# Performance work log

Hardware: AMD Instinct MI355X
Metric: run time of the kernel (lower is better)

The kernel has to match this reference:

```python
import jax, jax.numpy as jnp
import numpy as np

B, S, D, E, H = 65536, 4, 128, 128, 4
HD = E // H
EPS = 1e-5


def setup_inputs() -> dict:
    key = jax.random.key(0)
    ks = jax.random.split(key, 20)
    sc = 0.05
    return {
        'h0': jax.random.normal(ks[0], (B, D), jnp.float32),
        'h1': jax.random.normal(ks[1], (B, D), jnp.float32),
        'h2': jax.random.normal(ks[2], (B, D), jnp.float32),
        'h3': jax.random.normal(ks[3], (B, D), jnp.float32),
        'proj_w': jax.random.normal(ks[4], (S, D, E), jnp.float32) * sc,
        'proj_b': jax.random.normal(ks[5], (S, E), jnp.float32) * sc,
        'ctx_w': jax.random.normal(ks[6], (E,), jnp.float32) * sc,
        'ctx_b': jax.random.normal(ks[7], (), jnp.float32) * sc,
        'in_proj_w': jax.random.normal(ks[8], (E, 3 * E), jnp.float32) * sc,
        'in_proj_b': jax.random.normal(ks[9], (3 * E,), jnp.float32) * sc,
        'out_w': jax.random.normal(ks[10], (E, E), jnp.float32) * sc,
        'out_b': jax.random.normal(ks[11], (E,), jnp.float32) * sc,
        'gate_w': jax.random.normal(ks[12], (2 * E, E), jnp.float32) * sc,
        'gate_b': jax.random.normal(ks[13], (E,), jnp.float32) * sc,
        'pool_w': jax.random.normal(ks[14], (E,), jnp.float32) * sc,
        'pool_b': jax.random.normal(ks[15], (), jnp.float32) * sc,
        'ln_g': jnp.ones((E,), jnp.float32),
        'ln_b': jnp.zeros((E,), jnp.float32),
    }


def reference(h0, h1, h2, h3, proj_w, proj_b, ctx_w, ctx_b, in_proj_w, in_proj_b,
              out_w, out_b, gate_w, gate_b, pool_w, pool_b, ln_g, ln_b):
    hs = jnp.stack([h0, h1, h2, h3], axis=1)                      # [B,S,D]
    x = jnp.einsum('bsd,sde->bse', hs, proj_w) + proj_b           # [B,S,E]
    # context attention over sources
    cw = jax.nn.softmax(x @ ctx_w + ctx_b, axis=1)                # [B,S]
    context = jnp.einsum('bse,bs->be', x, cw)                     # [B,E]
    # single-query MHA: query=context, keys/vals=x
    wq, wk, wv = jnp.split(in_proj_w, 3, axis=1)
    bq, bk, bv = jnp.split(in_proj_b, 3)
    q = (context @ wq + bq).reshape(B, H, HD)
    k = (x @ wk + bk).reshape(B, S, H, HD)
    v = (x @ wv + bv).reshape(B, S, H, HD)
    scores = jnp.einsum('bhd,bshd->bhs', q, k) / jnp.sqrt(jnp.float32(HD))
    attn = jax.nn.softmax(scores, axis=-1)                        # [B,H,S]
    o = jnp.einsum('bhs,bshd->bhd', attn, v).reshape(B, E)
    attn_out = o @ out_w + out_b                                  # [B,E]
    attn_weights = jnp.mean(attn, axis=1)[:, None, :]             # [B,1,S] (avg heads)
    ao = jnp.broadcast_to(attn_out[:, None, :], (B, S, E))
    gate_in = jnp.concatenate([x, ao], axis=-1)                   # [B,S,2E]
    g = jax.nn.sigmoid(gate_in @ gate_w + gate_b)                 # [B,S,E]
    fused = g * ao + (1.0 - g) * x
    mu = fused.mean(axis=-1, keepdims=True)
    var = fused.var(axis=-1, keepdims=True)
    fused = (fused - mu) * jax.lax.rsqrt(var + EPS) * ln_g + ln_b
    pw = jax.nn.softmax(fused @ pool_w + pool_b, axis=1)          # [B,S]
    pooled = jnp.einsum('bse,bs->be', fused, pw)                  # [B,E]
    return pooled, attn_weights, g
```

## Files before the change

kernel.cpp:

```cpp
#include <hip/hip_runtime.h>
#include <hip/hip_bf16.h>

typedef unsigned short u16;
typedef unsigned int   u32;
typedef short  short8 __attribute__((ext_vector_type(8)));
typedef float  f32x4  __attribute__((ext_vector_type(4)));

#define NB   65536
#define ROWS 64
#define XP   136
#define OFF1 ((size_t)NB * 128)
#define OFF2 (OFF1 + (size_t)NB * 4)

__device__ __forceinline__ u16 f2bf(float f) {
  union { float f; u32 u; } v; v.f = f;
  return (u16)((v.u + 0x7FFFu + ((v.u >> 16) & 1u)) >> 16);
}
__device__ __forceinline__ float bf2f(u32 bits16) {
  union { u32 u; float f; } v; v.u = bits16 << 16; return v.f;
}
__device__ __forceinline__ u32 pk2(float a, float b) {
  return (u32)f2bf(a) | ((u32)f2bf(b) << 16);
}

__global__ void pack_w(const float* __restrict__ proj_w,
                       const float* __restrict__ in_proj_w,
                       const float* __restrict__ out_w,
                       const float* __restrict__ gate_w,
                       u16* __restrict__ wp) {
  int t = blockIdx.x * 256 + threadIdx.x;
  if (t >= 10 * 16384) return;
  int w = t >> 14, i = t & 16383;
  int nt = i >> 11, kt = (i >> 9) & 3, ln = (i >> 3) & 63, j = i & 7;
  int k = kt * 32 + ((ln >> 4) << 3) + j;
  int n = (nt << 4) + (ln & 15);
  float v;
  if (w < 4)       v = proj_w[((size_t)w << 14) + (k << 7) + n];
  else if (w < 7)  v = in_proj_w[k * 384 + ((w - 4) << 7) + n];
  else if (w == 7) v = out_w[(k << 7) + n];
  else             v = gate_w[(((w - 8) << 7) + k) * 128 + n];
  wp[t] = f2bf(v);
}

__device__ __forceinline__ short8 bfrag(const u16* __restrict__ wp, int w, int nt, int kt, int lane) {
  return *(const short8*)(wp + ((size_t)w << 14) + (size_t)((((nt << 2) + kt) << 6) + lane) * 8);
}

struct AF { short8 a[4]; };
__device__ __forceinline__ AF loadA(const u16 (*Ab)[XP], int row, int lgrp) {
  AF r;
  #pragma unroll
  for (int kt = 0; kt < 4; ++kt)
    r.a[kt] = *(const short8*)&Ab[row][kt * 32 + (lgrp << 3)];
  return r;
}
__device__ __forceinline__ f32x4 mmK128(const AF& A, const u16* __restrict__ wp, int w,
                                        int nt, int lane, float bias) {
  f32x4 acc = {bias, bias, bias, bias};
  #pragma unroll
  for (int kt = 0; kt < 4; ++kt)
    acc = __builtin_amdgcn_mfma_f32_16x16x32_bf16(A.a[kt], bfrag(wp, w, nt, kt, lane), acc, 0, 0, 0);
  return acc;
}

__global__ __launch_bounds__(256) void fused_k(
    const float* __restrict__ h0, const float* __restrict__ h1,
    const float* __restrict__ h2, const float* __restrict__ h3,
    const u16* __restrict__ wp,
    const float* __restrict__ proj_b, const float* __restrict__ ctx_w,
    const float* __restrict__ in_proj_b, const float* __restrict__ out_b,
    const float* __restrict__ gate_b, const float* __restrict__ pool_w,
    const float* __restrict__ ln_g, const float* __restrict__ ln_b,
    float* __restrict__ out) {
  __shared__ __align__(16) u16 xls[4][ROWS][XP];
  __shared__ __align__(16) u16 aux[ROWS][XP];
  __shared__ __align__(16) u16 aob[ROWS][XP];
  __shared__ float lgt[4][ROWS];
  __shared__ float scf[4][ROWS][4];
  __shared__ float lnr[ROWS][4][2];
  __shared__ float lgp[4][ROWS];
  __shared__ float lnw[3][128];

  const int tid  = threadIdx.x;
  const int lane = tid & 63;
  const int wr   = (tid >> 6) << 4;
  const int r0   = blockIdx.x * ROWS;
  const int lrow = lane & 15;
  const int lgrp = lane >> 4;
  const int crow0 = lgrp << 2;

  if (tid < 128) { lnw[0][tid] = pool_w[tid]; lnw[1][tid] = ln_g[tid]; lnw[2][tid] = ln_b[tid]; }

  const float* hp[4] = {h0, h1, h2, h3};

  #pragma unroll
  for (int s = 0; s < 4; ++s) {
    const float* __restrict__ hs = hp[s];
    #pragma unroll
    for (int i = 0; i < 8; ++i) {
      int f4 = i * 256 + tid;
      int row = f4 >> 5, c0 = (f4 & 31) << 2;
      const float4 v = *(const float4*)(hs + ((size_t)(r0 + row) << 7) + c0);
      *(uint2*)&aux[row][c0] = make_uint2(pk2(v.x, v.y), pk2(v.z, v.w));
    }
    __syncthreads();
    AF A = loadA(aux, wr + lrow, lgrp);
    float lp0 = 0, lp1 = 0, lp2 = 0, lp3 = 0;
    #pragma unroll
    for (int nt = 0; nt < 8; ++nt) {
      int n = (nt << 4) + lrow;
      f32x4 acc = mmK128(A, wp, s, nt, lane, proj_b[(s << 7) + n]);
      float cwn = ctx_w[n];
      lp0 += acc[0] * cwn; lp1 += acc[1] * cwn; lp2 += acc[2] * cwn; lp3 += acc[3] * cwn;
      xls[s][wr + crow0 + 0][n] = f2bf(acc[0]);
      xls[s][wr + crow0 + 1][n] = f2bf(acc[1]);
      xls[s][wr + crow0 + 2][n] = f2bf(acc[2]);
      xls[s][wr + crow0 + 3][n] = f2bf(acc[3]);
    }
    #pragma unroll
    for (int m = 1; m < 16; m <<= 1) {
      lp0 += __shfl_xor(lp0, m); lp1 += __shfl_xor(lp1, m);
      lp2 += __shfl_xor(lp2, m); lp3 += __shfl_xor(lp3, m);
    }
    if (lrow == 0) {
      lgt[s][wr + crow0 + 0] = lp0; lgt[s][wr + crow0 + 1] = lp1;
      lgt[s][wr + crow0 + 2] = lp2; lgt[s][wr + crow0 + 3] = lp3;
    }
    __syncthreads();
  }

  if (tid < ROWS) {
    float l0 = lgt[0][tid], l1 = lgt[1][tid], l2 = lgt[2][tid], l3 = lgt[3][tid];
    float mx = fmaxf(fmaxf(l0, l1), fmaxf(l2, l3));
    float e0 = __expf(l0 - mx), e1 = __expf(l1 - mx), e2 = __expf(l2 - mx), e3 = __expf(l3 - mx);
    float inv = 1.f / (e0 + e1 + e2 + e3);
    lgt[0][tid] = e0 * inv; lgt[1][tid] = e1 * inv; lgt[2][tid] = e2 * inv; lgt[3][tid] = e3 * inv;
  }
  __syncthreads();

  #pragma unroll
  for (int i = 0; i < 8; ++i) {
    int e4 = i * 256 + tid;
    int row = e4 >> 5, c0 = (e4 & 31) << 2;
    float c0v = 0, c1v = 0, c2v = 0, c3v = 0;
    #pragma unroll
    for (int s = 0; s < 4; ++s) {
      float cw = lgt[s][row];
      uint2 d = *(const uint2*)&xls[s][row][c0];
      c0v += cw * bf2f(d.x & 0xffff); c1v += cw * bf2f(d.x >> 16);
      c2v += cw * bf2f(d.y & 0xffff); c3v += cw * bf2f(d.y >> 16);
    }
    *(uint2*)&aux[row][c0] = make_uint2(pk2(c0v, c1v), pk2(c2v, c3v));
  }
  __syncthreads();

  {
    AF A = loadA(aux, wr + lrow, lgrp);
    #pragma unroll
    for (int nt = 0; nt < 8; ++nt) {
      int n = (nt << 4) + lrow;
      f32x4 acc = mmK128(A, wp, 4, nt, lane, in_proj_b[n]);
      #pragma unroll
      for (int j = 0; j < 4; ++j) aob[wr + crow0 + j][n] = f2bf(acc[j]);
    }
  }
  __syncthreads();

  #pragma unroll
  for (int s = 0; s < 4; ++s) {
    float sc[4][4] = {};
    AF A = loadA(xls[s], wr + lrow, lgrp);
    #pragma unroll
    for (int nt = 0; nt < 8; ++nt) {
      int n = (nt << 4) + lrow;
      f32x4 acc = mmK128(A, wp, 5, nt, lane, in_proj_b[128 + n]);
      #pragma unroll
      for (int j = 0; j < 4; ++j)
        sc[j][nt >> 1] += acc[j] * bf2f((u32)aob[wr + crow0 + j][n]);
    }
    #pragma unroll
    for (int m = 1; m < 16; m <<= 1)
      #pragma unroll
      for (int j = 0; j < 4; ++j)
        #pragma unroll
        for (int h = 0; h < 4; ++h)
          sc[j][h] += __shfl_xor(sc[j][h], m);
    #pragma unroll
    for (int h = 0; h < 4; ++h)
      if (lrow == h) {
        #pragma unroll
        for (int j = 0; j < 4; ++j) scf[s][wr + crow0 + j][h] = sc[j][h];
      }
  }
  __syncthreads();

  {
    int row = tid >> 2, h = tid & 3;
    const float scale = 0.17677669529663687f;
    float l0 = scf[0][row][h] * scale, l1 = scf[1][row][h] * scale;
    float l2 = scf[2][row][h] * scale, l3 = scf[3][row][h] * scale;
    float mx = fmaxf(fmaxf(l0, l1), fmaxf(l2, l3));
    float e0 = __expf(l0 - mx), e1 = __expf(l1 - mx), e2 = __expf(l2 - mx), e3 = __expf(l3 - mx);
    float inv = 1.f / (e0 + e1 + e2 + e3);
    scf[0][row][h] = e0 * inv; scf[1][row][h] = e1 * inv;
    scf[2][row][h] = e2 * inv; scf[3][row][h] = e3 * inv;
  }
  __syncthreads();
  {
    int row = tid >> 2, s = tid & 3;
    float m = 0.25f * (scf[s][row][0] + scf[s][row][1] + scf[s][row][2] + scf[s][row][3]);
    out[OFF1 + ((size_t)(r0 + row) << 2) + s] = m;
  }

  {
    float oa[8][4] = {};
    #pragma unroll
    for (int s = 0; s < 4; ++s) {
      AF A = loadA(xls[s], wr + lrow, lgrp);
      float aw[4][4];
      #pragma unroll
      for (int j = 0; j < 4; ++j)
        #pragma unroll
        for (int h = 0; h < 4; ++h) aw[j][h] = scf[s][wr + crow0 + j][h];
      #pragma unroll
      for (int nt = 0; nt < 8; ++nt) {
        int n = (nt << 4) + lrow;
        f32x4 acc = mmK128(A, wp, 6, nt, lane, in_proj_b[256 + n]);
        #pragma unroll
        for (int j = 0; j < 4; ++j) oa[nt][j] += aw[j][nt >> 1] * acc[j];
      }
    }
    #pragma unroll
    for (int nt = 0; nt < 8; ++nt) {
      int n = (nt << 4) + lrow;
      #pragma unroll
      for (int j = 0; j < 4; ++j) aux[wr + crow0 + j][n] = f2bf(oa[nt][j]);
    }
  }
  __syncthreads();

  {
    AF A = loadA(aux, wr + lrow, lgrp);
    #pragma unroll
    for (int nt = 0; nt < 8; ++nt) {
      int n = (nt << 4) + lrow;
      f32x4 acc = mmK128(A, wp, 7, nt, lane, out_b[n]);
      #pragma unroll
      for (int j = 0; j < 4; ++j) aob[wr + crow0 + j][n] = f2bf(acc[j]);
    }
  }
  __syncthreads();

  #pragma unroll 1
  for (int s = 0; s < 4; ++s) {
    {
      AF Ax = loadA(xls[s], wr + lrow, lgrp);
      AF Aa = loadA(aob, wr + lrow, lgrp);
      #pragma unroll
      for (int nt = 0; nt < 8; ++nt) {
        int n = (nt << 4) + lrow;
        float b = gate_b[n];
        f32x4 acc = {b, b, b, b};
        #pragma unroll
        for (int kt = 0; kt < 4; ++kt)
          acc = __builtin_amdgcn_mfma_f32_16x16x32_bf16(Ax.a[kt], bfrag(wp, 8, nt, kt, lane), acc, 0, 0, 0);
        #pragma unroll
        for (int kt = 0; kt < 4; ++kt)
          acc = __builtin_amdgcn_mfma_f32_16x16x32_bf16(Aa.a[kt], bfrag(wp, 9, nt, kt, lane), acc, 0, 0, 0);
        #pragma unroll
        for (int j = 0; j < 4; ++j) {
          float g = 1.f / (1.f + __expf(-acc[j]));
          out[OFF2 + (((size_t)(r0 + wr + crow0 + j) << 2) + s) * 128 + n] = g;
          aux[wr + crow0 + j][n] = f2bf(g);
        }
      }
    }
    __syncthreads();
    int row = tid >> 2, p = tid & 3, e0 = (tid & 3) << 5;
    float sum = 0, ss = 0;
    #pragma unroll
    for (int c = 0; c < 8; ++c) {
      int e = e0 + (c << 2);
      uint2 gd = *(const uint2*)&aux[row][e];
      uint2 ad = *(const uint2*)&aob[row][e];
      uint2 xd = *(const uint2*)&xls[s][row][e];
      float g0 = bf2f(gd.x & 0xffff), g1 = bf2f(gd.x >> 16), g2 = bf2f(gd.y & 0xffff), g3 = bf2f(gd.y >> 16);
      float a0 = bf2f(ad.x & 0xffff), a1 = bf2f(ad.x >> 16), a2 = bf2f(ad.y & 0xffff), a3 = bf2f(ad.y >> 16);
      float x0 = bf2f(xd.x & 0xffff), x1 = bf2f(xd.x >> 16), x2 = bf2f(xd.y & 0xffff), x3 = bf2f(xd.y >> 16);
      float f0 = g0 * a0 + (1.f - g0) * x0, f1 = g1 * a1 + (1.f - g1) * x1;
      float f2 = g2 * a2 + (1.f - g2) * x2, f3 = g3 * a3 + (1.f - g3) * x3;
      sum += f0 + f1 + f2 + f3;
      ss  += f0 * f0 + f1 * f1 + f2 * f2 + f3 * f3;
      *(uint2*)&xls[s][row][e] = make_uint2(pk2(f0, f1), pk2(f2, f3));
    }
    lnr[row][p][0] = sum; lnr[row][p][1] = ss;
    __syncthreads();
    float ts  = lnr[row][0][0] + lnr[row][1][0] + lnr[row][2][0] + lnr[row][3][0];
    float tss = lnr[row][0][1] + lnr[row][1][1] + lnr[row][2][1] + lnr[row][3][1];
    float mean = ts * 0.0078125f;
    float var  = tss * 0.0078125f - mean * mean;
    float rstd = rsqrtf(var + 1e-5f);
    float pp = 0;
    #pragma unroll
    for (int c = 0; c < 8; ++c) {
      int e = e0 + (c << 2);
      uint2 fd = *(const uint2*)&xls[s][row][e];
      float f0 = bf2f(fd.x & 0xffff), f1 = bf2f(fd.x >> 16), f2 = bf2f(fd.y & 0xffff), f3 = bf2f(fd.y >> 16);
      f0 = (f0 - mean) * rstd * lnw[1][e + 0] + lnw[2][e + 0];
      f1 = (f1 - mean) * rstd * lnw[1][e + 1] + lnw[2][e + 1];
      f2 = (f2 - mean) * rstd * lnw[1][e + 2] + lnw[2][e + 2];
      f3 = (f3 - mean) * rstd * lnw[1][e + 3] + lnw[2][e + 3];
      pp += f0 * lnw[0][e] + f1 * lnw[0][e + 1] + f2 * lnw[0][e + 2] + f3 * lnw[0][e + 3];
      *(uint2*)&xls[s][row][e] = make_uint2(pk2(f0, f1), pk2(f2, f3));
    }
    scf[0][row][p] = pp;
    __syncthreads();
    if (p == 0)
      lgp[s][row] = scf[0][row][0] + scf[0][row][1] + scf[0][row][2] + scf[0][row][3];
    __syncthreads();
  }

  if (tid < ROWS) {
    float l0 = lgp[0][tid], l1 = lgp[1][tid], l2 = lgp[2][tid], l3 = lgp[3][tid];
    float mx = fmaxf(fmaxf(l0, l1), fmaxf(l2, l3));
    float e0 = __expf(l0 - mx), e1 = __expf(l1 - mx), e2 = __expf(l2 - mx), e3 = __expf(l3 - mx);
    float inv = 1.f / (e0 + e1 + e2 + e3);
    lgp[0][tid] = e0 * inv; lgp[1][tid] = e1 * inv; lgp[2][tid] = e2 * inv; lgp[3][tid] = e3 * inv;
  }
  __syncthreads();
  #pragma unroll
  for (int i = 0; i < 8; ++i) {
    int e4 = i * 256 + tid;
    int row = e4 >> 5, c0 = (e4 & 31) << 2;
    float p0 = lgp[0][row], p1 = lgp[1][row], p2 = lgp[2][row], p3 = lgp[3][row];
    float r0v = 0, r1v = 0, r2v = 0, r3v = 0;
    #pragma unroll
    for (int s = 0; s < 4; ++s) {
      float pw = (s == 0) ? p0 : (s == 1) ? p1 : (s == 2) ? p2 : p3;
      uint2 d = *(const uint2*)&xls[s][row][c0];
      r0v += pw * bf2f(d.x & 0xffff); r1v += pw * bf2f(d.x >> 16);
      r2v += pw * bf2f(d.y & 0xffff); r3v += pw * bf2f(d.y >> 16);
    }
    float4 o4; o4.x = r0v; o4.y = r1v; o4.z = r2v; o4.w = r3v;
    *(float4*)(out + ((size_t)(r0 + row) << 7) + c0) = o4;
  }
}

extern "C" void kernel_launch(void* const* d_in, const int* in_sizes, int n_in,
                              void* d_out, int out_size, void* d_ws, size_t ws_size,
                              hipStream_t stream) {
  const float* h0        = (const float*)d_in[0];
  const float* h1        = (const float*)d_in[1];
  const float* h2        = (const float*)d_in[2];
  const float* h3        = (const float*)d_in[3];
  const float* proj_w    = (const float*)d_in[4];
  const float* proj_b    = (const float*)d_in[5];
  const float* ctx_w     = (const float*)d_in[6];
  const float* in_proj_w = (const float*)d_in[8];
  const float* in_proj_b = (const float*)d_in[9];
  const float* out_w     = (const float*)d_in[10];
  const float* out_b     = (const float*)d_in[11];
  const float* gate_w    = (const float*)d_in[12];
  const float* gate_b    = (const float*)d_in[13];
  const float* pool_w    = (const float*)d_in[14];
  const float* ln_g      = (const float*)d_in[16];
  const float* ln_b      = (const float*)d_in[17];
  u16* wp = (u16*)d_ws;

  pack_w<<<640, 256, 0, stream>>>(proj_w, in_proj_w, out_w, gate_w, wp);
  fused_k<<<NB / ROWS, 256, 0, stream>>>(h0, h1, h2, h3, wp,
                                         proj_b, ctx_w, in_proj_b, out_b, gate_b,
                                         pool_w, ln_g, ln_b, (float*)d_out);
}
```

Before: 211.3 us.

## Split output columns across two waves on 16-row tiles, keep operands in registers

The fused kernel now works on 16 rows per block with 128 threads. The two waves split the 128 output columns instead of the rows, so each weight fragment is loaded once and reused across the four sources. Source activations, q, and attention output stay in registers, and the gate, residual mix and layernorm are done on MFMA accumulators with cross-lane reductions rather than through shared-memory round trips. This cuts LDS traffic and barriers and may raise occupancy. In exchange, each block re-reads the full weight set for only 16 rows, and the code adds more cross-wave reductions and register pressure.

```diff
diff --git a/kernel.cpp b/kernel.cpp
--- a/kernel.cpp
+++ b/kernel.cpp
@@ -7,7 +7,7 @@
 typedef float  f32x4  __attribute__((ext_vector_type(4)));
 
 #define NB   65536
-#define ROWS 64
+#define ROWS 16
 #define XP   136
 #define OFF1 ((size_t)NB * 128)
 #define OFF2 (OFF1 + (size_t)NB * 4)
@@ -21,6 +21,11 @@
 }
 __device__ __forceinline__ u32 pk2(float a, float b) {
   return (u32)f2bf(a) | ((u32)f2bf(b) << 16);
+}
+__device__ __forceinline__ float red16(float v) {
+  v += __shfl_xor(v, 1); v += __shfl_xor(v, 2);
+  v += __shfl_xor(v, 4); v += __shfl_xor(v, 8);
+  return v;
 }
 
 __global__ void pack_w(const float* __restrict__ proj_w,
@@ -55,15 +60,15 @@
   return r;
 }
 __device__ __forceinline__ f32x4 mmK128(const AF& A, const u16* __restrict__ wp, int w,
-                                        int nt, int lane, float bias) {
+                                        int ntg, int lane, float bias) {
   f32x4 acc = {bias, bias, bias, bias};
   #pragma unroll
   for (int kt = 0; kt < 4; ++kt)
-    acc = __builtin_amdgcn_mfma_f32_16x16x32_bf16(A.a[kt], bfrag(wp, w, nt, kt, lane), acc, 0, 0, 0);
+    acc = __builtin_amdgcn_mfma_f32_16x16x32_bf16(A.a[kt], bfrag(wp, w, ntg, kt, lane), acc, 0, 0, 0);
   return acc;
 }
 
-__global__ __launch_bounds__(256) void fused_k(
+__global__ __launch_bounds__(128, 3) void fused_k(
     const float* __restrict__ h0, const float* __restrict__ h1,
     const float* __restrict__ h2, const float* __restrict__ h3,
     const u16* __restrict__ wp,
@@ -75,21 +80,19 @@
   __shared__ __align__(16) u16 xls[4][ROWS][XP];
   __shared__ __align__(16) u16 aux[ROWS][XP];
   __shared__ __align__(16) u16 aob[ROWS][XP];
-  __shared__ float lgt[4][ROWS];
+  __shared__ float lgt[4][2][ROWS];
   __shared__ float scf[4][ROWS][4];
-  __shared__ float lnr[ROWS][4][2];
-  __shared__ float lgp[4][ROWS];
-  __shared__ float lnw[3][128];
-
-  const int tid  = threadIdx.x;
-  const int lane = tid & 63;
-  const int wr   = (tid >> 6) << 4;
-  const int r0   = blockIdx.x * ROWS;
-  const int lrow = lane & 15;
-  const int lgrp = lane >> 4;
+  __shared__ float lnr[ROWS][2][2];
+  __shared__ float lgp2[4][ROWS][2];
+
+  const int tid   = threadIdx.x;
+  const int lane  = tid & 63;
+  const int wid   = tid >> 6;
+  const int nt0   = wid << 2;
+  const int r0    = blockIdx.x * ROWS;
+  const int lrow  = lane & 15;
+  const int lgrp  = lane >> 4;
   const int crow0 = lgrp << 2;
-
-  if (tid < 128) { lnw[0][tid] = pool_w[tid]; lnw[1][tid] = ln_g[tid]; lnw[2][tid] = ln_b[tid]; }
 
   const float* hp[4] = {h0, h1, h2, h3};
 
@@ -97,104 +100,130 @@
   for (int s = 0; s < 4; ++s) {
     const float* __restrict__ hs = hp[s];
     #pragma unroll
-    for (int i = 0; i < 8; ++i) {
-      int f4 = i * 256 + tid;
+    for (int i = 0; i < 4; ++i) {
+      int f4 = i * 128 + tid;
       int row = f4 >> 5, c0 = (f4 & 31) << 2;
       const float4 v = *(const float4*)(hs + ((size_t)(r0 + row) << 7) + c0);
-      *(uint2*)&aux[row][c0] = make_uint2(pk2(v.x, v.y), pk2(v.z, v.w));
-    }
-    __syncthreads();
-    AF A = loadA(aux, wr + lrow, lgrp);
-    float lp0 = 0, lp1 = 0, lp2 = 0, lp3 = 0;
-    #pragma unroll
-    for (int nt = 0; nt < 8; ++nt) {
-      int n = (nt << 4) + lrow;
-      f32x4 acc = mmK128(A, wp, s, nt, lane, proj_b[(s << 7) + n]);
+      *(uint2*)&xls[s][row][c0] = make_uint2(pk2(v.x, v.y), pk2(v.z, v.w));
+    }
+  }
+  __syncthreads();
+  AF Ah[4];
+  #pragma unroll
+  for (int s = 0; s < 4; ++s) Ah[s] = loadA(xls[s], lrow, lgrp);
+  __syncthreads();
+
+  #pragma unroll
+  for (int s = 0; s < 4; ++s) {
+    float lp[4] = {0.f, 0.f, 0.f, 0.f};
+    #pragma unroll
+    for (int nt = 0; nt < 4; ++nt) {
+      int ntg = nt0 + nt, n = (ntg << 4) + lrow;
+      f32x4 acc = mmK128(Ah[s], wp, s, ntg, lane, proj_b[(s << 7) + n]);
       float cwn = ctx_w[n];
-      lp0 += acc[0] * cwn; lp1 += acc[1] * cwn; lp2 += acc[2] * cwn; lp3 += acc[3] * cwn;
-      xls[s][wr + crow0 + 0][n] = f2bf(acc[0]);
-      xls[s][wr + crow0 + 1][n] = f2bf(acc[1]);
-      xls[s][wr + crow0 + 2][n] = f2bf(acc[2]);
-      xls[s][wr + crow0 + 3][n] = f2bf(acc[3]);
-    }
-    #pragma unroll
-    for (int m = 1; m < 16; m <<= 1) {
-      lp0 += __shfl_xor(lp0, m); lp1 += __shfl_xor(lp1, m);
-      lp2 += __shfl_xor(lp2, m); lp3 += __shfl_xor(lp3, m);
-    }
+      #pragma unroll
+      for (int j = 0; j < 4; ++j) {
+        lp[j] += acc[j] * cwn;
+        xls[s][crow0 + j][n] = f2bf(acc[j]);
+      }
+    }
+    #pragma unroll
+    for (int j = 0; j < 4; ++j) lp[j] = red16(lp[j]);
     if (lrow == 0) {
-      lgt[s][wr + crow0 + 0] = lp0; lgt[s][wr + crow0 + 1] = lp1;
-      lgt[s][wr + crow0 + 2] = lp2; lgt[s][wr + crow0 + 3] = lp3;
-    }
-    __syncthreads();
-  }
+      #pragma unroll
+      for (int j = 0; j < 4; ++j) lgt[s][wid][crow0 + j] = lp[j];
+    }
+  }
+  __syncthreads();
 
   if (tid < ROWS) {
-    float l0 = lgt[0][tid], l1 = lgt[1][tid], l2 = lgt[2][tid], l3 = lgt[3][tid];
+    float l0 = lgt[0][0][tid] + lgt[0][1][tid];
+    float l1 = lgt[1][0][tid] + lgt[1][1][tid];
+    float l2 = lgt[2][0][tid] + lgt[2][1][tid];
+    float l3 = lgt[3][0][tid] + lgt[3][1][tid];
     float mx = fmaxf(fmaxf(l0, l1), fmaxf(l2, l3));
     float e0 = __expf(l0 - mx), e1 = __expf(l1 - mx), e2 = __expf(l2 - mx), e3 = __expf(l3 - mx);
     float inv = 1.f / (e0 + e1 + e2 + e3);
-    lgt[0][tid] = e0 * inv; lgt[1][tid] = e1 * inv; lgt[2][tid] = e2 * inv; lgt[3][tid] = e3 * inv;
-  }
-  __syncthreads();
-
-  #pragma unroll
-  for (int i = 0; i < 8; ++i) {
-    int e4 = i * 256 + tid;
+    lgt[0][0][tid] = e0 * inv; lgt[1][0][tid] = e1 * inv;
+    lgt[2][0][tid] = e2 * inv; lgt[3][0][tid] = e3 * inv;
+  }
+  __syncthreads();
+
+  #pragma unroll
+  for (int i = 0; i < 4; ++i) {
+    int e4 = i * 128 + tid;
     int row = e4 >> 5, c0 = (e4 & 31) << 2;
-    float c0v = 0, c1v = 0, c2v = 0, c3v = 0;
+    float a0 = 0, a1 = 0, a2 = 0, a3 = 0;
     #pragma unroll
     for (int s = 0; s < 4; ++s) {
-      float cw = lgt[s][row];
+      float cw = lgt[s][0][row];
       uint2 d = *(const uint2*)&xls[s][row][c0];
-      c0v += cw * bf2f(d.x & 0xffff); c1v += cw * bf2f(d.x >> 16);
-      c2v += cw * bf2f(d.y & 0xffff); c3v += cw * bf2f(d.y >> 16);
-    }
-    *(uint2*)&aux[row][c0] = make_uint2(pk2(c0v, c1v), pk2(c2v, c3v));
-  }
-  __syncthreads();
-
+      a0 += cw * bf2f(d.x & 0xffff); a1 += cw * bf2f(d.x >> 16);
+      a2 += cw * bf2f(d.y & 0xffff); a3 += cw * bf2f(d.y >> 16);
+    }
+    *(uint2*)&aux[row][c0] = make_uint2(pk2(a0, a1), pk2(a2, a3));
+  }
+  __syncthreads();
+
+  AF Ax[4];
+  #pragma unroll
+  for (int s = 0; s < 4; ++s) Ax[s] = loadA(xls[s], lrow, lgrp);
+  float qf[4][4];
   {
-    AF A = loadA(aux, wr + lrow, lgrp);
-    #pragma unroll
-    for (int nt = 0; nt < 8; ++nt) {
-      int n = (nt << 4) + lrow;
-      f32x4 acc = mmK128(A, wp, 4, nt, lane, in_proj_b[n]);
-      #pragma unroll
-      for (int j = 0; j < 4; ++j) aob[wr + crow0 + j][n] = f2bf(acc[j]);
-    }
-  }
-  __syncthreads();
-
-  #pragma unroll
-  for (int s = 0; s < 4; ++s) {
-    float sc[4][4] = {};
-    AF A = loadA(xls[s], wr + lrow, lgrp);
-    #pragma unroll
-    for (int nt = 0; nt < 8; ++nt) {
-      int n = (nt << 4) + lrow;
-      f32x4 acc = mmK128(A, wp, 5, nt, lane, in_proj_b[128 + n]);
+    AF Ac = loadA(aux, lrow, lgrp);
+    #pragma unroll
+    for (int nt = 0; nt < 4; ++nt) {
+      int ntg = nt0 + nt, n = (ntg << 4) + lrow;
+      f32x4 acc = mmK128(Ac, wp, 4, ntg, lane, in_proj_b[n]);
+      #pragma unroll
+      for (int j = 0; j < 4; ++j) qf[nt][j] = acc[j];
+    }
+  }
+
+  {
+    float sc[4][4][2] = {};
+    #pragma unroll
+    for (int nt = 0; nt < 4; ++nt) {
+      int ntg = nt0 + nt, n = (ntg << 4) + lrow;
+      const int hh = (ntg >> 1) & 1;
+      float bk = in_proj_b[128 + n];
+      f32x4 ak[4];
+      #pragma unroll
+      for (int s = 0; s < 4; ++s) ak[s] = (f32x4){bk, bk, bk, bk};
+      #pragma unroll
+      for (int kt = 0; kt < 4; ++kt) {
+        short8 bf = bfrag(wp, 5, ntg, kt, lane);
+        #pragma unroll
+        for (int s = 0; s < 4; ++s)
+          ak[s] = __builtin_amdgcn_mfma_f32_16x16x32_bf16(Ax[s].a[kt], bf, ak[s], 0, 0, 0);
+      }
+      #pragma unroll
+      for (int s = 0; s < 4; ++s)
+        #pragma unroll
+        for (int j = 0; j < 4; ++j)
+          sc[s][j][hh] += ak[s][j] * qf[nt][j];
+    }
+    #pragma unroll
+    for (int s = 0; s < 4; ++s)
       #pragma unroll
       for (int j = 0; j < 4; ++j)
-        sc[j][nt >> 1] += acc[j] * bf2f((u32)aob[wr + crow0 + j][n]);
-    }
-    #pragma unroll
-    for (int m = 1; m < 16; m <<= 1)
-      #pragma unroll
-      for (int j = 0; j < 4; ++j)
-        #pragma unroll
-        for (int h = 0; h < 4; ++h)
-          sc[j][h] += __shfl_xor(sc[j][h], m);
-    #pragma unroll
-    for (int h = 0; h < 4; ++h)
-      if (lrow == h) {
-        #pragma unroll
-        for (int j = 0; j < 4; ++j) scf[s][wr + crow0 + j][h] = sc[j][h];
-      }
-  }
-  __syncthreads();
-
-  {
+        #pragma unroll
+        for (int hh = 0; hh < 2; ++hh)
+          sc[s][j][hh] = red16(sc[s][j][hh]);
+    #pragma unroll
+    for (int s = 0; s < 4; ++s)
+      #pragma unroll
+      for (int hh = 0; hh < 2; ++hh) {
+        int h = (wid << 1) + hh;
+        if (lrow == h) {
+          #pragma unroll
+          for (int j = 0; j < 4; ++j) scf[s][crow0 + j][h] = sc[s][j][hh];
+        }
+      }
+  }
+  __syncthreads();
+
+  if (tid < 64) {
     int row = tid >> 2, h = tid & 3;
     const float scale = 0.17677669529663687f;
     float l0 = scf[0][row][h] * scale, l1 = scf[1][row][h] * scale;
@@ -206,137 +235,161 @@
     scf[2][row][h] = e2 * inv; scf[3][row][h] = e3 * inv;
   }
   __syncthreads();
-  {
+  if (tid < 64) {
     int row = tid >> 2, s = tid & 3;
     float m = 0.25f * (scf[s][row][0] + scf[s][row][1] + scf[s][row][2] + scf[s][row][3]);
     out[OFF1 + ((size_t)(r0 + row) << 2) + s] = m;
   }
 
   {
-    float oa[8][4] = {};
+    float aw[4][4][2];
+    #pragma unroll
+    for (int s = 0; s < 4; ++s)
+      #pragma unroll
+      for (int j = 0; j < 4; ++j)
+        #pragma unroll
+        for (int hh = 0; hh < 2; ++hh)
+          aw[s][j][hh] = scf[s][crow0 + j][(wid << 1) + hh];
+    float oa[4][4] = {};
+    #pragma unroll
+    for (int nt = 0; nt < 4; ++nt) {
+      int ntg = nt0 + nt, n = (ntg << 4) + lrow;
+      const int hh = (ntg >> 1) & 1;
+      float bv = in_proj_b[256 + n];
+      f32x4 av[4];
+      #pragma unroll
+      for (int s = 0; s < 4; ++s) av[s] = (f32x4){bv, bv, bv, bv};
+      #pragma unroll
+      for (int kt = 0; kt < 4; ++kt) {
+        short8 bf = bfrag(wp, 6, ntg, kt, lane);
+        #pragma unroll
+        for (int s = 0; s < 4; ++s)
+          av[s] = __builtin_amdgcn_mfma_f32_16x16x32_bf16(Ax[s].a[kt], bf, av[s], 0, 0, 0);
+      }
+      #pragma unroll
+      for (int s = 0; s < 4; ++s)
+        #pragma unroll
+        for (int j = 0; j < 4; ++j)
+          oa[nt][j] += aw[s][j][hh] * av[s][j];
+    }
+    #pragma unroll
+    for (int nt = 0; nt < 4; ++nt) {
+      int n = ((nt0 + nt) << 4) + lrow;
+      #pragma unroll
+      for (int j = 0; j < 4; ++j) aux[crow0 + j][n] = f2bf(oa[nt][j]);
+    }
+  }
+  __syncthreads();
+
+  float aoreg[4][4];
+  {
+    AF Ao = loadA(aux, lrow, lgrp);
+    #pragma unroll
+    for (int nt = 0; nt < 4; ++nt) {
+      int ntg = nt0 + nt, n = (ntg << 4) + lrow;
+      f32x4 acc = mmK128(Ao, wp, 7, ntg, lane, out_b[n]);
+      #pragma unroll
+      for (int j = 0; j < 4; ++j) {
+        aoreg[nt][j] = acc[j];
+        aob[crow0 + j][n] = f2bf(acc[j]);
+      }
+    }
+  }
+  __syncthreads();
+
+  {
+    AF Aa = loadA(aob, lrow, lgrp);
+    float lng[4], lnb[4], pwv[4], gbv[4];
+    #pragma unroll
+    for (int nt = 0; nt < 4; ++nt) {
+      int n = ((nt0 + nt) << 4) + lrow;
+      lng[nt] = ln_g[n]; lnb[nt] = ln_b[n]; pwv[nt] = pool_w[n]; gbv[nt] = gate_b[n];
+    }
     #pragma unroll
     for (int s = 0; s < 4; ++s) {
-      AF A = loadA(xls[s], wr + lrow, lgrp);
-      float aw[4][4];
-      #pragma unroll
-      for (int j = 0; j < 4; ++j)
-        #pragma unroll
-        for (int h = 0; h < 4; ++h) aw[j][h] = scf[s][wr + crow0 + j][h];
-      #pragma unroll
-      for (int nt = 0; nt < 8; ++nt) {
-        int n = (nt << 4) + lrow;
-        f32x4 acc = mmK128(A, wp, 6, nt, lane, in_proj_b[256 + n]);
-        #pragma unroll
-        for (int j = 0; j < 4; ++j) oa[nt][j] += aw[j][nt >> 1] * acc[j];
-      }
-    }
-    #pragma unroll
-    for (int nt = 0; nt < 8; ++nt) {
-      int n = (nt << 4) + lrow;
-      #pragma unroll
-      for (int j = 0; j < 4; ++j) aux[wr + crow0 + j][n] = f2bf(oa[nt][j]);
-    }
-  }
-  __syncthreads();
-
-  {
-    AF A = loadA(aux, wr + lrow, lgrp);
-    #pragma unroll
-    for (int nt = 0; nt < 8; ++nt) {
-      int n = (nt << 4) + lrow;
-      f32x4 acc = mmK128(A, wp, 7, nt, lane, out_b[n]);
-      #pragma unroll
-      for (int j = 0; j < 4; ++j) aob[wr + crow0 + j][n] = f2bf(acc[j]);
-    }
-  }
-  __syncthreads();
-
-  #pragma unroll 1
-  for (int s = 0; s < 4; ++s) {
-    {
-      AF Ax = loadA(xls[s], wr + lrow, lgrp);
-      AF Aa = loadA(aob, wr + lrow, lgrp);
-      #pragma unroll
-      for (int nt = 0; nt < 8; ++nt) {
-        int n = (nt << 4) + lrow;
-        float b = gate_b[n];
-        f32x4 acc = {b, b, b, b};
+      float fr[4][4];
+      #pragma unroll
+      for (int nt = 0; nt < 4; ++nt) {
+        int ntg = nt0 + nt, n = (ntg << 4) + lrow;
+        f32x4 acc = {gbv[nt], gbv[nt], gbv[nt], gbv[nt]};
         #pragma unroll
         for (int kt = 0; kt < 4; ++kt)
-          acc = __builtin_amdgcn_mfma_f32_16x16x32_bf16(Ax.a[kt], bfrag(wp, 8, nt, kt, lane), acc, 0, 0, 0);
+          acc = __builtin_amdgcn_mfma_f32_16x16x32_bf16(Ax[s].a[kt], bfrag(wp, 8, ntg, kt, lane), acc, 0, 0, 0);
         #pragma unroll
         for (int kt = 0; kt < 4; ++kt)
-          acc = __builtin_amdgcn_mfma_f32_16x16x32_bf16(Aa.a[kt], bfrag(wp, 9, nt, kt, lane), acc, 0, 0, 0);
+          acc = __builtin_amdgcn_mfma_f32_16x16x32_bf16(Aa.a[kt], bfrag(wp, 9, ntg, kt, lane), acc, 0, 0, 0);
         #pragma unroll
         for (int j = 0; j < 4; ++j) {
           float g = 1.f / (1.f + __expf(-acc[j]));
-          out[OFF2 + (((size_t)(r0 + wr + crow0 + j) << 2) + s) * 128 + n] = g;
-          aux[wr + crow0 + j][n] = f2bf(g);
+          out[OFF2 + (((size_t)(r0 + crow0 + j) << 2) + s) * 128 + n] = g;
+          float xv = bf2f((u32)xls[s][crow0 + j][n]);
+          fr[nt][j] = g * aoreg[nt][j] + (1.f - g) * xv;
         }
       }
-    }
-    __syncthreads();
-    int row = tid >> 2, p = tid & 3, e0 = (tid & 3) << 5;
-    float sum = 0, ss = 0;
-    #pragma unroll
-    for (int c = 0; c < 8; ++c) {
-      int e = e0 + (c << 2);
-      uint2 gd = *(const uint2*)&aux[row][e];
-      uint2 ad = *(const uint2*)&aob[row][e];
-      uint2 xd = *(const uint2*)&xls[s][row][e];
-      float g0 = bf2f(gd.x & 0xffff), g1 = bf2f(gd.x >> 16), g2 = bf2f(gd.y & 0xffff), g3 = bf2f(gd.y >> 16);
-      float a0 = bf2f(ad.x & 0xffff), a1 = bf2f(ad.x >> 16), a2 = bf2f(ad.y & 0xffff), a3 = bf2f(ad.y >> 16);
-      float x0 = bf2f(xd.x & 0xffff), x1 = bf2f(xd.x >> 16), x2 = bf2f(xd.y & 0xffff), x3 = bf2f(xd.y >> 16);
-      float f0 = g0 * a0 + (1.f - g0) * x0, f1 = g1 * a1 + (1.f - g1) * x1;
-      float f2 = g2 * a2 + (1.f - g2) * x2, f3 = g3 * a3 + (1.f - g3) * x3;
-      sum += f0 + f1 + f2 + f3;
-      ss  += f0 * f0 + f1 * f1 + f2 * f2 + f3 * f3;
-      *(uint2*)&xls[s][row][e] = make_uint2(pk2(f0, f1), pk2(f2, f3));
-    }
-    lnr[row][p][0] = sum; lnr[row][p][1] = ss;
-    __syncthreads();
-    float ts  = lnr[row][0][0] + lnr[row][1][0] + lnr[row][2][0] + lnr[row][3][0];
-    float tss = lnr[row][0][1] + lnr[row][1][1] + lnr[row][2][1] + lnr[row][3][1];
-    float mean = ts * 0.0078125f;
-    float var  = tss * 0.0078125f - mean * mean;
-    float rstd = rsqrtf(var + 1e-5f);
-    float pp = 0;
-    #pragma unroll
-    for (int c = 0; c < 8; ++c) {
-      int e = e0 + (c << 2);
-      uint2 fd = *(const uint2*)&xls[s][row][e];
-      float f0 = bf2f(fd.x & 0xffff), f1 = bf2f(fd.x >> 16), f2 = bf2f(fd.y & 0xffff), f3 = bf2f(fd.y >> 16);
-      f0 = (f0 - mean) * rstd * lnw[1][e + 0] + lnw[2][e + 0];
-      f1 = (f1 - mean) * rstd * lnw[1][e + 1] + lnw[2][e + 1];
-      f2 = (f2 - mean) * rstd * lnw[1][e + 2] + lnw[2][e + 2];
-      f3 = (f3 - mean) * rstd * lnw[1][e + 3] + lnw[2][e + 3];
-      pp += f0 * lnw[0][e] + f1 * lnw[0][e + 1] + f2 * lnw[0][e + 2] + f3 * lnw[0][e + 3];
-      *(uint2*)&xls[s][row][e] = make_uint2(pk2(f0, f1), pk2(f2, f3));
-    }
-    scf[0][row][p] = pp;
-    __syncthreads();
-    if (p == 0)
-      lgp[s][row] = scf[0][row][0] + scf[0][row][1] + scf[0][row][2] + scf[0][row][3];
-    __syncthreads();
+      float sm[4] = {0, 0, 0, 0}, sq[4] = {0, 0, 0, 0};
+      #pragma unroll
+      for (int nt = 0; nt < 4; ++nt)
+        #pragma unroll
+        for (int j = 0; j < 4; ++j) {
+          sm[j] += fr[nt][j];
+          sq[j] += fr[nt][j] * fr[nt][j];
+        }
+      #pragma unroll
+      for (int j = 0; j < 4; ++j) { sm[j] = red16(sm[j]); sq[j] = red16(sq[j]); }
+      if (lrow == 0) {
+        #pragma unroll
+        for (int j = 0; j < 4; ++j) {
+          lnr[crow0 + j][wid][0] = sm[j];
+          lnr[crow0 + j][wid][1] = sq[j];
+        }
+      }
+      __syncthreads();
+      float pp[4] = {0, 0, 0, 0};
+      #pragma unroll
+      for (int j = 0; j < 4; ++j) {
+        float ts = lnr[crow0 + j][0][0] + lnr[crow0 + j][1][0];
+        float tq = lnr[crow0 + j][0][1] + lnr[crow0 + j][1][1];
+        float mean = ts * 0.0078125f;
+        float var  = tq * 0.0078125f - mean * mean;
+        float rstd = rsqrtf(var + 1e-5f);
+        #pragma unroll
+        for (int nt = 0; nt < 4; ++nt) {
+          int n = ((nt0 + nt) << 4) + lrow;
+          float fn = (fr[nt][j] - mean) * rstd * lng[nt] + lnb[nt];
+          xls[s][crow0 + j][n] = f2bf(fn);
+          pp[j] += fn * pwv[nt];
+        }
+      }
+      #pragma unroll
+      for (int j = 0; j < 4; ++j) pp[j] = red16(pp[j]);
+      if (lrow == 0) {
+        #pragma unroll
+        for (int j = 0; j < 4; ++j) lgp2[s][crow0 + j][wid] = pp[j];
+      }
+      __syncthreads();
+    }
   }
 
   if (tid < ROWS) {
-    float l0 = lgp[0][tid], l1 = lgp[1][tid], l2 = lgp[2][tid], l3 = lgp[3][tid];
+    float l0 = lgp2[0][tid][0] + lgp2[0][tid][1];
+    float l1 = lgp2[1][tid][0] + lgp2[1][tid][1];
+    float l2 = lgp2[2][tid][0] + lgp2[2][tid][1];
+    float l3 = lgp2[3][tid][0] + lgp2[3][tid][1];
     float mx = fmaxf(fmaxf(l0, l1), fmaxf(l2, l3));
     float e0 = __expf(l0 - mx), e1 = __expf(l1 - mx), e2 = __expf(l2 - mx), e3 = __expf(l3 - mx);
     float inv = 1.f / (e0 + e1 + e2 + e3);
-    lgp[0][tid] = e0 * inv; lgp[1][tid] = e1 * inv; lgp[2][tid] = e2 * inv; lgp[3][tid] = e3 * inv;
-  }
-  __syncthreads();
-  #pragma unroll
-  for (int i = 0; i < 8; ++i) {
-    int e4 = i * 256 + tid;
+    lgp2[0][tid][0] = e0 * inv; lgp2[1][tid][0] = e1 * inv;
+    lgp2[2][tid][0] = e2 * inv; lgp2[3][tid][0] = e3 * inv;
+  }
+  __syncthreads();
+  #pragma unroll
+  for (int i = 0; i < 4; ++i) {
+    int e4 = i * 128 + tid;
     int row = e4 >> 5, c0 = (e4 & 31) << 2;
-    float p0 = lgp[0][row], p1 = lgp[1][row], p2 = lgp[2][row], p3 = lgp[3][row];
     float r0v = 0, r1v = 0, r2v = 0, r3v = 0;
     #pragma unroll
     for (int s = 0; s < 4; ++s) {
-      float pw = (s == 0) ? p0 : (s == 1) ? p1 : (s == 2) ? p2 : p3;
+      float pw = lgp2[s][row][0];
       uint2 d = *(const uint2*)&xls[s][row][c0];
       r0v += pw * bf2f(d.x & 0xffff); r1v += pw * bf2f(d.x >> 16);
       r2v += pw * bf2f(d.y & 0xffff); r3v += pw * bf2f(d.y >> 16);
@@ -368,7 +421,7 @@
   u16* wp = (u16*)d_ws;
 
   pack_w<<<640, 256, 0, stream>>>(proj_w, in_proj_w, out_w, gate_w, wp);
-  fused_k<<<NB / ROWS, 256, 0, stream>>>(h0, h1, h2, h3, wp,
+  fused_k<<<NB / ROWS, 128, 0, stream>>>(h0, h1, h2, h3, wp,
                                          proj_b, ctx_w, in_proj_b, out_b, gate_b,
                                          pool_w, ln_g, ln_b, (float*)d_out);
 }
```

After: 431.2 us. +104.1%, slower.
